# Kernel tuning notes

Measured on AMD Instinct MI355X. Metric: run time of the kernel, lower is better.

The kernel has to match this reference:

```python
import jax, jax.numpy as jnp
import numpy as np

N_LEVELS = 16
F = 2
LOG2_3D = 15
LOG2_4D = 22
B_PTS = 262144
PRIMES = [1, 2654435761, 805459861, 3674653429]

# per-level resolutions: floor(base * b**i), b = exp((log(fin)-log(base))/(L-1))
_b = np.exp((np.log(512.0) - np.log(16.0)) / (N_LEVELS - 1))
_bt = np.exp((np.log(32.0) - np.log(2.0)) / (N_LEVELS - 1))
RES = np.floor(16.0 * _b ** np.arange(N_LEVELS)).astype(np.float32)
RES_T = np.floor(2.0 * _bt ** np.arange(N_LEVELS)).astype(np.float32)

# corner offsets; first coordinate is the outermost bit (matches torch interp ordering)
OFF3 = np.array([[i, j, k] for i in (0, 1) for j in (0, 1) for k in (0, 1)], dtype=np.int32)
OFF4 = np.array([[i, j, k, l] for i in (0, 1) for j in (0, 1) for k in (0, 1) for l in (0, 1)], dtype=np.int32)


def _hash(coords, log2_size):
    # coords: [..., D] int32 (non-negative). Low bits of (c_i * p_i) are wrap-invariant,
    # and the final mask keeps < 32 bits, so uint32 math matches torch's int64 hash.
    c = coords.astype(jnp.uint32)
    h = c[..., 0] * jnp.uint32(PRIMES[0] & 0xFFFFFFFF)
    for i in range(1, coords.shape[-1]):
        h = h ^ (c[..., i] * jnp.uint32(PRIMES[i] & 0xFFFFFFFF))
    return (h & jnp.uint32((1 << log2_size) - 1)).astype(jnp.int32)


def _level_embed(x, table, box_min, box_max, res_vec, log2_size, offsets):
    # x: [B, D]; table: [T, F]; res_vec: [D]; offsets: [2^D, D]
    grid = (box_max - box_min) / res_vec                       # [D] voxel size
    xc = jnp.clip(x, box_min, box_max)
    bl = jnp.floor((xc - box_min) / grid)                      # [B, D] bottom-left idx
    vmin = bl * grid + box_min                                 # voxel_min_vertex
    w = (x - vmin) / grid                                      # interp weights (uses unclamped x, as in torch)
    idx = bl.astype(jnp.int32)[:, None, :] + offsets[None]     # [B, 2^D, D]
    v = table[_hash(idx, log2_size)]                           # [B, 2^D, F] irregular gather
    D = x.shape[-1]
    for d in range(D):                                         # multilinear reduce, dim 0 outermost
        n = v.shape[1] // 2
        wd = w[:, d][:, None, None]
        v = v[:, :n] * (1 - wd) + v[:, n:] * wd
    return v[:, 0]                                             # [B, F]


def _multires_embed(x, tables, box_min, box_max, res_levels, log2_size, offsets):
    outs = [_level_embed(x, tables[i], box_min, box_max,
                         jnp.asarray(res_levels[i], dtype=jnp.float32),
                         log2_size, jnp.asarray(offsets))
            for i in range(N_LEVELS)]
    return jnp.concatenate(outs, axis=-1)                      # [B, L*F]


def _forward(x, emb4d, emb3d):
    bmin4 = jnp.zeros(4, jnp.float32)
    bmax4 = jnp.ones(4, jnp.float32)
    bmin3, bmax3 = bmin4[:3], bmax4[:3]
    res4 = np.stack([RES, RES, RES, RES_T], axis=1)            # [L, 4]
    res3 = np.stack([RES, RES, RES], axis=1)                   # [L, 3]
    e4 = _multires_embed(x, emb4d, bmin4, bmax4, res4, LOG2_4D, OFF4)
    e3 = _multires_embed(x[:, :3], emb3d, bmin3, bmax3, res3, LOG2_3D, OFF3)
    embedded = e4 + e3                                         # modus='add'
    keep4 = jnp.all((x >= bmin4) & (x <= bmax4), axis=-1)
    keep3 = jnp.all((x[:, :3] >= bmin3) & (x[:, :3] <= bmax3), axis=-1)
    return embedded, keep4 & keep3


def setup_inputs() -> dict:
    key = jax.random.key(0)
    k1, k2, k3 = jax.random.split(key, 3)
    x = jax.random.uniform(k1, (B_PTS, 4), dtype=jnp.float32)
    emb4d = jax.random.uniform(k2, (N_LEVELS, 2 ** LOG2_4D, F), dtype=jnp.float32,
                               minval=-1e-4, maxval=1e-4)
    emb3d = jax.random.uniform(k3, (N_LEVELS, 2 ** LOG2_3D, F), dtype=jnp.float32,
                               minval=-1e-4, maxval=1e-4)
    return {"x": x, "emb4d": emb4d, "emb3d": emb3d}


def reference(x, emb4d, emb3d):
    return _forward(x, emb4d, emb3d)
```

## Files before the change

kernel.cpp:

```cpp
#include <hip/hip_runtime.h>
#include <math.h>
#include <stdint.h>

#define B_PTS   262144
#define NLEV    16
#define MASK4   ((1u << 22) - 1u)
#define MASK3   ((1u << 15) - 1u)
#define P1      2654435761u
#define P2      805459861u
#define P3      3674653429u

#define LSH     3
#define NSHL    (NLEV - LSH)
#define NCHUNK  256

typedef float f32x4 __attribute__((ext_vector_type(4)));

struct LevelParams {
    float res[NLEV];
    float rest[NLEV];
};

struct PtState {
    uint32_t a;
    uint32_t t1e, t1o, t2e, t2o, t3e, t3o;
    float w0, w1, w2, w3;
};

__device__ inline PtState mk_fast(float xx, float xy, float xz, float xw,
                                  float R, float Rt)
{
    PtState st;
    const float xd[4] = { xx, xy, xz, xw };
    const float rv[4] = { R, R, R, Rt };
    uint32_t tt[4][2]; float ww[4];
    #pragma unroll
    for (int d = 0; d < 4; ++d) {
        float xc = fminf(fmaxf(xd[d], 0.0f), 1.0f);
        float bl = floorf(xc * rv[d]);
        float w  = fmaf(xd[d], rv[d], -bl);
        uint32_t bi = (uint32_t)(int)bl;
        uint32_t prime = (d == 0) ? 1u : (d == 1) ? P1 : (d == 2) ? P2 : P3;
        tt[d][0] = bi * prime;
        tt[d][1] = tt[d][0] + prime;
        ww[d] = w;
    }
    st.a   = tt[0][0];
    st.t1e = tt[1][0]; st.t1o = tt[1][1];
    st.t2e = tt[2][0]; st.t2o = tt[2][1];
    st.t3e = tt[3][0]; st.t3o = tt[3][1];
    st.w0 = ww[0]; st.w1 = ww[1]; st.w2 = ww[2]; st.w3 = ww[3];
    return st;
}

__device__ inline uint32_t bfr(float v) {
    uint32_t u = __float_as_uint(v);
    u += 0x7FFFu + ((u >> 16) & 1u);
    return u >> 16;
}

__global__ __launch_bounds__(256)
void k_shard(const float4* __restrict__ x,
             const float2* __restrict__ emb4d,
             uint32_t* __restrict__ ws2, LevelParams lp)
{
    const int bid   = blockIdx.x;
    const int s     = bid & 7;
    const int rest  = bid >> 3;
    const int chunk = rest & (NCHUNK - 1);
    const int levi  = rest >> 8;
    const int lev   = LSH + levi;
    const uint32_t sh = (uint32_t)s;

    const float2* tab4 = emb4d + ((size_t)lev << 22);
    const float R = lp.res[lev], Rt = lp.rest[lev];
    const int pbase = chunk * 1024 + threadIdx.x;
    uint32_t* dst = ws2 + (size_t)(levi * 8 + s) * B_PTS + pbase;

    #pragma unroll
    for (int i = 0; i < 4; ++i) {
        f32x4 xr = __builtin_nontemporal_load(
            reinterpret_cast<const f32x4*>(&x[pbase + i * 256]));
        PtState st = mk_fast(xr.x, xr.y, xr.z, xr.w, R, Rt);

        const float w1e = 1.0f - st.w1, w2e = 1.0f - st.w2, w3e = 1.0f - st.w3;
        const float q00 = w1e * w2e, q01 = w1e * st.w2,
                    q10 = st.w1 * w2e, q11 = st.w1 * st.w2;
        const float wc[8] = { q00 * w3e, q00 * st.w3, q01 * w3e, q01 * st.w3,
                              q10 * w3e, q10 * st.w3, q11 * w3e, q11 * st.w3 };
        const float wx0 = 1.0f - st.w0, wx1 = st.w0;
        const uint32_t a0 = st.a, a1 = st.a + 1u;

        float vx[16], vy[16], wt[16];
        #pragma unroll
        for (int c = 0; c < 16; ++c) {
            const uint32_t E = ((c & 8) ? st.t1o : st.t1e) ^
                               ((c & 4) ? st.t2o : st.t2e) ^
                               ((c & 2) ? st.t3o : st.t3e) ^
                               ((c & 1) ? a1 : a0);
            const uint32_t h = E & MASK4;
            const bool act = (h >> 19) == sh;
            float fx = 0.0f, fy = 0.0f;
            if (act) {
                float2 v = tab4[h];
                fx = v.x; fy = v.y;
            }
            vx[c] = fx; vy[c] = fy;
            wt[c] = wc[c >> 1] * ((c & 1) ? wx1 : wx0);
        }

        float ex = 0.0f, ey = 0.0f;
        #pragma unroll
        for (int c = 0; c < 16; ++c) {
            ex = fmaf(vx[c], wt[c], ex);
            ey = fmaf(vy[c], wt[c], ey);
        }

        uint32_t pk = bfr(ex) | (bfr(ey) << 16);
        __builtin_nontemporal_store(pk, dst + i * 256);
    }
}

__global__ __launch_bounds__(256)
void k_final(const float4* __restrict__ x,
             const float2* __restrict__ emb4d,
             const float2* __restrict__ emb3d,
             const uint32_t* __restrict__ ws2,
             float* __restrict__ out, float* __restrict__ keep,
             LevelParams lp)
{
    __shared__ float tile[256 * 17];
    const int t    = threadIdx.x;
    const int p    = blockIdx.x * 256 + t;
    const int lev0 = blockIdx.y * 8;

    const float4 xv = x[p];

    for (int li8 = 0; li8 < 8; ++li8) {
        const int lev = lev0 + li8;
        PtState st = mk_fast(xv.x, xv.y, xv.z, xv.w, lp.res[lev], lp.rest[lev]);
        const uint32_t a0 = st.a, a1 = st.a + 1u;
        const float wx[2] = { 1.0f - st.w0, st.w0 };
        const float wy[2] = { 1.0f - st.w1, st.w1 };
        const float wz[2] = { 1.0f - st.w2, st.w2 };
        const float wwv[2] = { 1.0f - st.w3, st.w3 };

        float ex = 0.0f, ey = 0.0f;

        if (lev >= LSH) {
            const int li = lev - LSH;
            #pragma unroll
            for (int s2 = 0; s2 < 8; ++s2) {
                uint32_t w = ws2[(size_t)(li * 8 + s2) * B_PTS + p];
                ex += __uint_as_float(w << 16);
                ey += __uint_as_float(w & 0xFFFF0000u);
            }
        }

        {
            const float2* tab3 = emb3d + ((size_t)lev << 15);
            #pragma unroll
            for (int c = 0; c < 8; ++c) {
                uint32_t E = ((c & 2) ? st.t1o : st.t1e) ^
                             ((c & 1) ? st.t2o : st.t2e);
                uint32_t h = (E ^ ((c & 4) ? a1 : a0)) & MASK3;
                float wtv = wx[(c >> 2) & 1] * wy[(c >> 1) & 1] * wz[c & 1];
                float2 v = tab3[h];
                ex = fmaf(v.x, wtv, ex);
                ey = fmaf(v.y, wtv, ey);
            }
        }

        if (lev < LSH) {
            const float2* tab4 = emb4d + ((size_t)lev << 22);
            #pragma unroll
            for (int c = 0; c < 16; ++c) {
                uint32_t E = ((c & 4) ? st.t1o : st.t1e) ^
                             ((c & 2) ? st.t2o : st.t2e) ^
                             ((c & 1) ? st.t3o : st.t3e);
                uint32_t h = (E ^ ((c & 8) ? a1 : a0)) & MASK4;
                float wtv = wx[(c >> 3) & 1] * wy[(c >> 2) & 1] *
                            wz[(c >> 1) & 1] * wwv[c & 1];
                float2 v = tab4[h];
                ex = fmaf(v.x, wtv, ex);
                ey = fmaf(v.y, wtv, ey);
            }
        }

        tile[t * 17 + 2 * li8]     = ex;
        tile[t * 17 + 2 * li8 + 1] = ey;
    }

    __syncthreads();

    float* ob = out + (size_t)blockIdx.x * (256 * 32) + lev0 * 2;
    #pragma unroll
    for (int k = 0; k < 16; ++k) {
        int idx = k * 256 + t;
        int row = idx >> 4, col = idx & 15;
        ob[(size_t)row * 32 + col] = tile[row * 17 + col];
    }

    if (blockIdx.y == 0) {
        bool k4 = (xv.x >= 0.0f) && (xv.x <= 1.0f) &&
                  (xv.y >= 0.0f) && (xv.y <= 1.0f) &&
                  (xv.z >= 0.0f) && (xv.z <= 1.0f) &&
                  (xv.w >= 0.0f) && (xv.w <= 1.0f);
        keep[p] = k4 ? 1.0f : 0.0f;
    }
}

__global__ __launch_bounds__(256)
void embed_all(const float4* __restrict__ x,
               const float2* __restrict__ emb4d,
               const float2* __restrict__ emb3d,
               float* __restrict__ out,
               float* __restrict__ keep,
               LevelParams lp)
{
    __shared__ float tile[16 * 33];
    const int t = threadIdx.x;
    const int pl = t & 15;
    const int lev = t >> 4;
    const int pbase = blockIdx.x * 16;

    const float4 xv = x[pbase + pl];
    PtState st = mk_fast(xv.x, xv.y, xv.z, xv.w, lp.res[lev], lp.rest[lev]);
    const uint32_t a0 = st.a, a1 = st.a + 1u;
    const float wx[2] = { 1.0f - st.w0, st.w0 };
    const float wy[2] = { 1.0f - st.w1, st.w1 };
    const float wz[2] = { 1.0f - st.w2, st.w2 };
    const float wwv[2] = { 1.0f - st.w3, st.w3 };
    float ex = 0.0f, ey = 0.0f;

    const float2* tab4 = emb4d + ((size_t)lev << 22);
    #pragma unroll
    for (int c = 0; c < 16; ++c) {
        uint32_t E = ((c & 4) ? st.t1o : st.t1e) ^ ((c & 2) ? st.t2o : st.t2e) ^
                     ((c & 1) ? st.t3o : st.t3e);
        uint32_t h = (E ^ ((c & 8) ? a1 : a0)) & MASK4;
        float wt = wx[(c >> 3) & 1] * wy[(c >> 2) & 1] *
                   wz[(c >> 1) & 1] * wwv[c & 1];
        float2 v = tab4[h];
        ex = fmaf(v.x, wt, ex);
        ey = fmaf(v.y, wt, ey);
    }
    const float2* tab3 = emb3d + ((size_t)lev << 15);
    #pragma unroll
    for (int c = 0; c < 8; ++c) {
        uint32_t E = ((c & 2) ? st.t1o : st.t1e) ^ ((c & 1) ? st.t2o : st.t2e);
        uint32_t h = (E ^ ((c & 4) ? a1 : a0)) & MASK3;
        float wt = wx[(c >> 2) & 1] * wy[(c >> 1) & 1] * wz[c & 1];
        float2 v = tab3[h];
        ex = fmaf(v.x, wt, ex);
        ey = fmaf(v.y, wt, ey);
    }

    tile[pl * 33 + 2 * lev]     = ex;
    tile[pl * 33 + 2 * lev + 1] = ey;
    __syncthreads();
    {
        int pw = t >> 4;
        int cw = (2 * t) & 31;
        float2 v = make_float2(tile[pw * 33 + cw], tile[pw * 33 + cw + 1]);
        *reinterpret_cast<float2*>(out + (size_t)pbase * 32 + 2 * t) = v;
    }
    if (t < 16) {
        const float4 xk = x[pbase + t];
        bool k4 = (xk.x >= 0.0f) && (xk.x <= 1.0f) &&
                  (xk.y >= 0.0f) && (xk.y <= 1.0f) &&
                  (xk.z >= 0.0f) && (xk.z <= 1.0f) &&
                  (xk.w >= 0.0f) && (xk.w <= 1.0f);
        keep[pbase + t] = k4 ? 1.0f : 0.0f;
    }
}

extern "C" void kernel_launch(void* const* d_in, const int* in_sizes, int n_in,
                              void* d_out, int out_size, void* d_ws, size_t ws_size,
                              hipStream_t stream)
{
    const float4* x     = (const float4*)d_in[0];
    const float2* emb4d = (const float2*)d_in[1];
    const float2* emb3d = (const float2*)d_in[2];
    float* out  = (float*)d_out;
    float* keep = out + (size_t)B_PTS * 32;

    LevelParams lp;
    const double b  = exp((log(512.0) - log(16.0)) / 15.0);
    const double bt = exp((log(32.0)  - log(2.0))  / 15.0);
    for (int i = 0; i < NLEV; ++i) {
        lp.res[i]  = (float)floor(16.0 * pow(b,  (double)i));
        lp.rest[i] = (float)floor(2.0  * pow(bt, (double)i));
    }

    const size_t ws2_bytes = (size_t)NSHL * 8 * B_PTS * 4;

    if (ws_size >= ws2_bytes && d_ws != nullptr) {
        uint32_t* ws2 = (uint32_t*)d_ws;
        k_shard<<<NSHL * NCHUNK * 8,        256, 0, stream>>>(x, emb4d, ws2, lp);
        k_final<<<dim3(B_PTS / 256, 2),     256, 0, stream>>>(x, emb4d, emb3d,
                                                              ws2, out, keep, lp);
    } else {
        embed_all<<<B_PTS / 16, 256, 0, stream>>>(x, emb4d, emb3d, out, keep, lp);
    }
}
```

Measured before the change: 512.8 us.

## Software-pipeline shard gathers across points and split final kernel into four level groups

The shard kernel now issues gathers for the next point before reducing the previous one, using double-buffered register state and sched_barriers, so gather latency overlaps with arithmetic. Gathers are grouped by shared E so both x-corners are fetched under one predicate, and launch bounds now request 3 waves per SIMD. The final kernel splits levels into 4 groups of 4 instead of 2 of 8 to expose more blocks. The double-buffered state raises register pressure, which could cause spills under the occupancy hint.

```diff
diff --git a/kernel.cpp b/kernel.cpp
--- a/kernel.cpp
+++ b/kernel.cpp
@@ -27,8 +27,8 @@
     float w0, w1, w2, w3;
 };
 
-__device__ inline PtState mk_fast(float xx, float xy, float xz, float xw,
-                                  float R, float Rt)
+__device__ __forceinline__ PtState mk_fast(float xx, float xy, float xz, float xw,
+                                           float R, float Rt)
 {
     PtState st;
     const float xd[4] = { xx, xy, xz, xw };
@@ -53,13 +53,64 @@
     return st;
 }
 
-__device__ inline uint32_t bfr(float v) {
+__device__ __forceinline__ uint32_t bfr(float v) {
     uint32_t u = __float_as_uint(v);
     u += 0x7FFFu + ((u >> 16) & 1u);
     return u >> 16;
 }
 
-__global__ __launch_bounds__(256)
+struct CBuf {
+    float vx0[8], vy0[8], vx1[8], vy1[8];
+    float wtp[8];
+    float wx0, wx1;
+};
+
+__device__ __forceinline__ void issue_point(const float2* __restrict__ tab4,
+                                            f32x4 xr, float R, float Rt,
+                                            uint32_t sh, CBuf& b)
+{
+    PtState st = mk_fast(xr.x, xr.y, xr.z, xr.w, R, Rt);
+    const float w1e = 1.0f - st.w1, w2e = 1.0f - st.w2, w3e = 1.0f - st.w3;
+    const float q00 = w1e * w2e, q01 = w1e * st.w2,
+                q10 = st.w1 * w2e, q11 = st.w1 * st.w2;
+    b.wtp[0] = q00 * w3e; b.wtp[1] = q00 * st.w3;
+    b.wtp[2] = q01 * w3e; b.wtp[3] = q01 * st.w3;
+    b.wtp[4] = q10 * w3e; b.wtp[5] = q10 * st.w3;
+    b.wtp[6] = q11 * w3e; b.wtp[7] = q11 * st.w3;
+    b.wx0 = 1.0f - st.w0; b.wx1 = st.w0;
+    const uint32_t a0 = st.a, a1 = a0 + 1u;
+
+    #pragma unroll
+    for (int pp = 0; pp < 8; ++pp) {
+        uint32_t E = ((pp & 4) ? st.t1o : st.t1e) ^
+                     ((pp & 2) ? st.t2o : st.t2e) ^
+                     ((pp & 1) ? st.t3o : st.t3e);
+        E &= MASK4;
+        float2 v0 = make_float2(0.0f, 0.0f);
+        float2 v1 = make_float2(0.0f, 0.0f);
+        if ((E >> 19) == sh) {
+            v0 = tab4[E ^ a0];
+            v1 = tab4[E ^ a1];
+        }
+        b.vx0[pp] = v0.x; b.vy0[pp] = v0.y;
+        b.vx1[pp] = v1.x; b.vy1[pp] = v1.y;
+    }
+}
+
+__device__ __forceinline__ uint32_t consume_point(const CBuf& b)
+{
+    float ex = 0.0f, ey = 0.0f;
+    #pragma unroll
+    for (int pp = 0; pp < 8; ++pp) {
+        float u0 = b.wtp[pp] * b.wx0;
+        float u1 = b.wtp[pp] * b.wx1;
+        ex = fmaf(b.vx1[pp], u1, fmaf(b.vx0[pp], u0, ex));
+        ey = fmaf(b.vy1[pp], u1, fmaf(b.vy0[pp], u0, ey));
+    }
+    return bfr(ex) | (bfr(ey) << 16);
+}
+
+__global__ __launch_bounds__(256, 3)
 void k_shard(const float4* __restrict__ x,
              const float2* __restrict__ emb4d,
              uint32_t* __restrict__ ws2, LevelParams lp)
@@ -77,48 +128,24 @@
     const int pbase = chunk * 1024 + threadIdx.x;
     uint32_t* dst = ws2 + (size_t)(levi * 8 + s) * B_PTS + pbase;
 
-    #pragma unroll
-    for (int i = 0; i < 4; ++i) {
-        f32x4 xr = __builtin_nontemporal_load(
-            reinterpret_cast<const f32x4*>(&x[pbase + i * 256]));
-        PtState st = mk_fast(xr.x, xr.y, xr.z, xr.w, R, Rt);
-
-        const float w1e = 1.0f - st.w1, w2e = 1.0f - st.w2, w3e = 1.0f - st.w3;
-        const float q00 = w1e * w2e, q01 = w1e * st.w2,
-                    q10 = st.w1 * w2e, q11 = st.w1 * st.w2;
-        const float wc[8] = { q00 * w3e, q00 * st.w3, q01 * w3e, q01 * st.w3,
-                              q10 * w3e, q10 * st.w3, q11 * w3e, q11 * st.w3 };
-        const float wx0 = 1.0f - st.w0, wx1 = st.w0;
-        const uint32_t a0 = st.a, a1 = st.a + 1u;
-
-        float vx[16], vy[16], wt[16];
-        #pragma unroll
-        for (int c = 0; c < 16; ++c) {
-            const uint32_t E = ((c & 8) ? st.t1o : st.t1e) ^
-                               ((c & 4) ? st.t2o : st.t2e) ^
-                               ((c & 2) ? st.t3o : st.t3e) ^
-                               ((c & 1) ? a1 : a0);
-            const uint32_t h = E & MASK4;
-            const bool act = (h >> 19) == sh;
-            float fx = 0.0f, fy = 0.0f;
-            if (act) {
-                float2 v = tab4[h];
-                fx = v.x; fy = v.y;
-            }
-            vx[c] = fx; vy[c] = fy;
-            wt[c] = wc[c >> 1] * ((c & 1) ? wx1 : wx0);
-        }
-
-        float ex = 0.0f, ey = 0.0f;
-        #pragma unroll
-        for (int c = 0; c < 16; ++c) {
-            ex = fmaf(vx[c], wt[c], ex);
-            ey = fmaf(vy[c], wt[c], ey);
-        }
-
-        uint32_t pk = bfr(ex) | (bfr(ey) << 16);
-        __builtin_nontemporal_store(pk, dst + i * 256);
-    }
+    f32x4 x0 = __builtin_nontemporal_load(reinterpret_cast<const f32x4*>(&x[pbase]));
+    f32x4 x1 = __builtin_nontemporal_load(reinterpret_cast<const f32x4*>(&x[pbase + 256]));
+    f32x4 x2 = __builtin_nontemporal_load(reinterpret_cast<const f32x4*>(&x[pbase + 512]));
+    f32x4 x3 = __builtin_nontemporal_load(reinterpret_cast<const f32x4*>(&x[pbase + 768]));
+
+    CBuf A, B;
+    issue_point(tab4, x0, R, Rt, sh, A);
+    __builtin_amdgcn_sched_barrier(0);
+    issue_point(tab4, x1, R, Rt, sh, B);
+    __builtin_amdgcn_sched_barrier(0);
+    __builtin_nontemporal_store(consume_point(A), dst);
+    issue_point(tab4, x2, R, Rt, sh, A);
+    __builtin_amdgcn_sched_barrier(0);
+    __builtin_nontemporal_store(consume_point(B), dst + 256);
+    issue_point(tab4, x3, R, Rt, sh, B);
+    __builtin_amdgcn_sched_barrier(0);
+    __builtin_nontemporal_store(consume_point(A), dst + 512);
+    __builtin_nontemporal_store(consume_point(B), dst + 768);
 }
 
 __global__ __launch_bounds__(256)
@@ -129,15 +156,16 @@
              float* __restrict__ out, float* __restrict__ keep,
              LevelParams lp)
 {
-    __shared__ float tile[256 * 17];
+    __shared__ float tile[256 * 9];
     const int t    = threadIdx.x;
     const int p    = blockIdx.x * 256 + t;
-    const int lev0 = blockIdx.y * 8;
+    const int lev0 = blockIdx.y * 4;
 
     const float4 xv = x[p];
 
-    for (int li8 = 0; li8 < 8; ++li8) {
-        const int lev = lev0 + li8;
+    #pragma unroll
+    for (int l4 = 0; l4 < 4; ++l4) {
+        const int lev = lev0 + l4;
         PtState st = mk_fast(xv.x, xv.y, xv.z, xv.w, lp.res[lev], lp.rest[lev]);
         const uint32_t a0 = st.a, a1 = st.a + 1u;
         const float wx[2] = { 1.0f - st.w0, st.w0 };
@@ -187,18 +215,18 @@
             }
         }
 
-        tile[t * 17 + 2 * li8]     = ex;
-        tile[t * 17 + 2 * li8 + 1] = ey;
+        tile[t * 9 + 2 * l4]     = ex;
+        tile[t * 9 + 2 * l4 + 1] = ey;
     }
 
     __syncthreads();
 
     float* ob = out + (size_t)blockIdx.x * (256 * 32) + lev0 * 2;
     #pragma unroll
-    for (int k = 0; k < 16; ++k) {
+    for (int k = 0; k < 8; ++k) {
         int idx = k * 256 + t;
-        int row = idx >> 4, col = idx & 15;
-        ob[(size_t)row * 32 + col] = tile[row * 17 + col];
+        int row = idx >> 3, col = idx & 7;
+        ob[(size_t)row * 32 + col] = tile[row * 9 + col];
     }
 
     if (blockIdx.y == 0) {
@@ -297,9 +325,9 @@
 
     if (ws_size >= ws2_bytes && d_ws != nullptr) {
         uint32_t* ws2 = (uint32_t*)d_ws;
-        k_shard<<<NSHL * NCHUNK * 8,        256, 0, stream>>>(x, emb4d, ws2, lp);
-        k_final<<<dim3(B_PTS / 256, 2),     256, 0, stream>>>(x, emb4d, emb3d,
-                                                              ws2, out, keep, lp);
+        k_shard<<<NSHL * NCHUNK * 8,    256, 0, stream>>>(x, emb4d, ws2, lp);
+        k_final<<<dim3(B_PTS / 256, 4), 256, 0, stream>>>(x, emb4d, emb3d,
+                                                          ws2, out, keep, lp);
     } else {
         embed_all<<<B_PTS / 16, 256, 0, stream>>>(x, emb4d, emb3d, out, keep, lp);
     }
```

Result: faster. 483.9 us (-5.6%).

## Pair adjacent x-corner hash lookups into one 16-byte load and rebalance level split

Applied to the files above, without the earlier changes.

Corners that differ only in the first coordinate hash to neighbouring table entries when the base index is even, so each pair is now fetched with one aligned float4 load plus an extra float2 load only when the base is odd. This applies to the sharded 4D kernel, the 3D tables, and the unsharded low 4D levels. The number of levels handled directly in the final kernel goes from 3 to 4, and the final kernel now covers 4 levels per block over 4 y-blocks instead of 8 over 2. The goal is fewer gather transactions, at the cost of wider loads, extra selects, and a different balance of work between the two kernels.

```diff
diff --git a/kernel.cpp b/kernel.cpp
--- a/kernel.cpp
+++ b/kernel.cpp
@@ -10,7 +10,7 @@
 #define P2      805459861u
 #define P3      3674653429u
 
-#define LSH     3
+#define LSH     4
 #define NSHL    (NLEV - LSH)
 #define NCHUNK  256
 
@@ -27,8 +27,8 @@
     float w0, w1, w2, w3;
 };
 
-__device__ inline PtState mk_fast(float xx, float xy, float xz, float xw,
-                                  float R, float Rt)
+__device__ __forceinline__ PtState mk_fast(float xx, float xy, float xz, float xw,
+                                           float R, float Rt)
 {
     PtState st;
     const float xd[4] = { xx, xy, xz, xw };
@@ -53,7 +53,7 @@
     return st;
 }
 
-__device__ inline uint32_t bfr(float v) {
+__device__ __forceinline__ uint32_t bfr(float v) {
     uint32_t u = __float_as_uint(v);
     u += 0x7FFFu + ((u >> 16) & 1u);
     return u >> 16;
@@ -89,31 +89,41 @@
         const float wc[8] = { q00 * w3e, q00 * st.w3, q01 * w3e, q01 * st.w3,
                               q10 * w3e, q10 * st.w3, q11 * w3e, q11 * st.w3 };
         const float wx0 = 1.0f - st.w0, wx1 = st.w0;
-        const uint32_t a0 = st.a, a1 = st.a + 1u;
-
-        float vx[16], vy[16], wt[16];
+        const uint32_t a0 = st.a, a1 = a0 + 1u;
+        const bool odd = (a0 & 1u) != 0u;
+
+        float4   q[8];
+        float2   e2[8];
+        uint32_t hib = 0;
+
         #pragma unroll
-        for (int c = 0; c < 16; ++c) {
-            const uint32_t E = ((c & 8) ? st.t1o : st.t1e) ^
-                               ((c & 4) ? st.t2o : st.t2e) ^
-                               ((c & 2) ? st.t3o : st.t3e) ^
-                               ((c & 1) ? a1 : a0);
-            const uint32_t h = E & MASK4;
-            const bool act = (h >> 19) == sh;
-            float fx = 0.0f, fy = 0.0f;
-            if (act) {
-                float2 v = tab4[h];
-                fx = v.x; fy = v.y;
-            }
-            vx[c] = fx; vy[c] = fy;
-            wt[c] = wc[c >> 1] * ((c & 1) ? wx1 : wx0);
+        for (int pp = 0; pp < 8; ++pp) {
+            uint32_t E = (((pp & 4) ? st.t1o : st.t1e) ^
+                          ((pp & 2) ? st.t2o : st.t2e) ^
+                          ((pp & 1) ? st.t3o : st.t3e)) & MASK4;
+            uint32_t h0 = E ^ a0;
+            hib |= (h0 & 1u) << pp;
+            float4 qq = make_float4(0.0f, 0.0f, 0.0f, 0.0f);
+            float2 ee = make_float2(0.0f, 0.0f);
+            const bool act = (E >> 19) == sh;
+            if (act)
+                qq = *reinterpret_cast<const float4*>(tab4 + (h0 & ~1u));
+            if (act && odd)
+                ee = tab4[E ^ a1];
+            q[pp] = qq; e2[pp] = ee;
         }
 
         float ex = 0.0f, ey = 0.0f;
         #pragma unroll
-        for (int c = 0; c < 16; ++c) {
-            ex = fmaf(vx[c], wt[c], ex);
-            ey = fmaf(vy[c], wt[c], ey);
+        for (int pp = 0; pp < 8; ++pp) {
+            const bool hi = (hib >> pp) & 1u;
+            float c0x = hi ? q[pp].z : q[pp].x;
+            float c0y = hi ? q[pp].w : q[pp].y;
+            float c1x = odd ? e2[pp].x : (hi ? q[pp].x : q[pp].z);
+            float c1y = odd ? e2[pp].y : (hi ? q[pp].y : q[pp].w);
+            float u0 = wc[pp] * wx0, u1 = wc[pp] * wx1;
+            ex = fmaf(c0x, u0, fmaf(c1x, u1, ex));
+            ey = fmaf(c0y, u0, fmaf(c1y, u1, ey));
         }
 
         uint32_t pk = bfr(ex) | (bfr(ey) << 16);
@@ -129,18 +139,20 @@
              float* __restrict__ out, float* __restrict__ keep,
              LevelParams lp)
 {
-    __shared__ float tile[256 * 17];
+    __shared__ float tile[256 * 9];
     const int t    = threadIdx.x;
     const int p    = blockIdx.x * 256 + t;
-    const int lev0 = blockIdx.y * 8;
+    const int lev0 = blockIdx.y * 4;
 
     const float4 xv = x[p];
 
-    for (int li8 = 0; li8 < 8; ++li8) {
-        const int lev = lev0 + li8;
+    #pragma unroll
+    for (int l4 = 0; l4 < 4; ++l4) {
+        const int lev = lev0 + l4;
         PtState st = mk_fast(xv.x, xv.y, xv.z, xv.w, lp.res[lev], lp.rest[lev]);
         const uint32_t a0 = st.a, a1 = st.a + 1u;
-        const float wx[2] = { 1.0f - st.w0, st.w0 };
+        const bool odd = (a0 & 1u) != 0u;
+        const float wx0 = 1.0f - st.w0, wx1 = st.w0;
         const float wy[2] = { 1.0f - st.w1, st.w1 };
         const float wz[2] = { 1.0f - st.w2, st.w2 };
         const float wwv[2] = { 1.0f - st.w3, st.w3 };
@@ -160,45 +172,56 @@
         {
             const float2* tab3 = emb3d + ((size_t)lev << 15);
             #pragma unroll
-            for (int c = 0; c < 8; ++c) {
-                uint32_t E = ((c & 2) ? st.t1o : st.t1e) ^
-                             ((c & 1) ? st.t2o : st.t2e);
-                uint32_t h = (E ^ ((c & 4) ? a1 : a0)) & MASK3;
-                float wtv = wx[(c >> 2) & 1] * wy[(c >> 1) & 1] * wz[c & 1];
-                float2 v = tab3[h];
-                ex = fmaf(v.x, wtv, ex);
-                ey = fmaf(v.y, wtv, ey);
+            for (int pp = 0; pp < 4; ++pp) {
+                uint32_t E = (((pp & 2) ? st.t1o : st.t1e) ^
+                              ((pp & 1) ? st.t2o : st.t2e)) & MASK3;
+                uint32_t h0 = E ^ a0;
+                float4 qq = *reinterpret_cast<const float4*>(tab3 + (h0 & ~1u));
+                float2 ee = make_float2(0.0f, 0.0f);
+                if (odd) ee = tab3[E ^ a1];
+                const bool hi = (h0 & 1u) != 0u;
+                float c0x = hi ? qq.z : qq.x, c0y = hi ? qq.w : qq.y;
+                float c1x = odd ? ee.x : (hi ? qq.x : qq.z);
+                float c1y = odd ? ee.y : (hi ? qq.y : qq.w);
+                float wp = wy[(pp >> 1) & 1] * wz[pp & 1];
+                ex = fmaf(c0x, wp * wx0, fmaf(c1x, wp * wx1, ex));
+                ey = fmaf(c0y, wp * wx0, fmaf(c1y, wp * wx1, ey));
             }
         }
 
         if (lev < LSH) {
             const float2* tab4 = emb4d + ((size_t)lev << 22);
             #pragma unroll
-            for (int c = 0; c < 16; ++c) {
-                uint32_t E = ((c & 4) ? st.t1o : st.t1e) ^
-                             ((c & 2) ? st.t2o : st.t2e) ^
-                             ((c & 1) ? st.t3o : st.t3e);
-                uint32_t h = (E ^ ((c & 8) ? a1 : a0)) & MASK4;
-                float wtv = wx[(c >> 3) & 1] * wy[(c >> 2) & 1] *
-                            wz[(c >> 1) & 1] * wwv[c & 1];
-                float2 v = tab4[h];
-                ex = fmaf(v.x, wtv, ex);
-                ey = fmaf(v.y, wtv, ey);
+            for (int pp = 0; pp < 8; ++pp) {
+                uint32_t E = (((pp & 4) ? st.t1o : st.t1e) ^
+                              ((pp & 2) ? st.t2o : st.t2e) ^
+                              ((pp & 1) ? st.t3o : st.t3e)) & MASK4;
+                uint32_t h0 = E ^ a0;
+                float4 qq = *reinterpret_cast<const float4*>(tab4 + (h0 & ~1u));
+                float2 ee = make_float2(0.0f, 0.0f);
+                if (odd) ee = tab4[E ^ a1];
+                const bool hi = (h0 & 1u) != 0u;
+                float c0x = hi ? qq.z : qq.x, c0y = hi ? qq.w : qq.y;
+                float c1x = odd ? ee.x : (hi ? qq.x : qq.z);
+                float c1y = odd ? ee.y : (hi ? qq.y : qq.w);
+                float wp = wy[(pp >> 2) & 1] * wz[(pp >> 1) & 1] * wwv[pp & 1];
+                ex = fmaf(c0x, wp * wx0, fmaf(c1x, wp * wx1, ex));
+                ey = fmaf(c0y, wp * wx0, fmaf(c1y, wp * wx1, ey));
             }
         }
 
-        tile[t * 17 + 2 * li8]     = ex;
-        tile[t * 17 + 2 * li8 + 1] = ey;
+        tile[t * 9 + 2 * l4]     = ex;
+        tile[t * 9 + 2 * l4 + 1] = ey;
     }
 
     __syncthreads();
 
     float* ob = out + (size_t)blockIdx.x * (256 * 32) + lev0 * 2;
     #pragma unroll
-    for (int k = 0; k < 16; ++k) {
+    for (int k = 0; k < 8; ++k) {
         int idx = k * 256 + t;
-        int row = idx >> 4, col = idx & 15;
-        ob[(size_t)row * 32 + col] = tile[row * 17 + col];
+        int row = idx >> 3, col = idx & 7;
+        ob[(size_t)row * 32 + col] = tile[row * 9 + col];
     }
 
     if (blockIdx.y == 0) {
@@ -297,9 +320,9 @@
 
     if (ws_size >= ws2_bytes && d_ws != nullptr) {
         uint32_t* ws2 = (uint32_t*)d_ws;
-        k_shard<<<NSHL * NCHUNK * 8,        256, 0, stream>>>(x, emb4d, ws2, lp);
-        k_final<<<dim3(B_PTS / 256, 2),     256, 0, stream>>>(x, emb4d, emb3d,
-                                                              ws2, out, keep, lp);
+        k_shard<<<NSHL * NCHUNK * 8,    256, 0, stream>>>(x, emb4d, ws2, lp);
+        k_final<<<dim3(B_PTS / 256, 4), 256, 0, stream>>>(x, emb4d, emb3d,
+                                                          ws2, out, keep, lp);
     } else {
         embed_all<<<B_PTS / 16, 256, 0, stream>>>(x, emb4d, emb3d, out, keep, lp);
     }
```

Result: faster. 477.6 us (-6.9%).
